# Kernel tuning notes

Measured on AMD Instinct MI355X. Metric: run time of the kernel, lower is better.

The kernel has to match this reference:

```python
import jax, jax.numpy as jnp
import numpy as np

DIM = 512
NUM_HEADS = 8
HEAD_DIM = DIM // NUM_HEADS
SCALE = HEAD_DIM ** -0.5


def setup_inputs() -> dict:
    key = jax.random.key(0)
    ks = jax.random.split(key, 10)
    B, Sq, Skv = 4, 2048, 2048
    std = DIM ** -0.5
    return {
        "x1": jax.random.normal(ks[0], (B, Sq, DIM), jnp.float32),
        "x2": jax.random.normal(ks[1], (B, Skv, DIM), jnp.float32),
        "Wq": jax.random.normal(ks[2], (DIM, DIM), jnp.float32) * std,
        "bq": jax.random.normal(ks[3], (DIM,), jnp.float32) * 0.02,
        "Wk": jax.random.normal(ks[4], (DIM, DIM), jnp.float32) * std,
        "bk": jax.random.normal(ks[5], (DIM,), jnp.float32) * 0.02,
        "Wv": jax.random.normal(ks[6], (DIM, DIM), jnp.float32) * std,
        "bv": jax.random.normal(ks[7], (DIM,), jnp.float32) * 0.02,
        "Wo": jax.random.normal(ks[8], (DIM, DIM), jnp.float32) * std,
        "bo": jax.random.normal(ks[9], (DIM,), jnp.float32) * 0.02,
    }


def reference(x1, x2, Wq, bq, Wk, bk, Wv, bv, Wo, bo):
    B, Sq, _ = x1.shape
    Skv = x2.shape[1]
    # Linear projections (torch nn.Linear: x @ W.T + b)
    Q = (x1 @ Wq.T + bq).reshape(B, Sq, NUM_HEADS, HEAD_DIM)
    K = (x2 @ Wk.T + bk).reshape(B, Skv, NUM_HEADS, HEAD_DIM)
    V = (x2 @ Wv.T + bv).reshape(B, Skv, NUM_HEADS, HEAD_DIM)
    # [B, H, Sq, Skv]
    attn = jnp.einsum("bqhd,bkhd->bhqk", Q, K) * SCALE
    attn = jax.nn.softmax(attn, axis=-1)  # dropout is identity in eval mode
    out = jnp.einsum("bhqk,bkhd->bqhd", attn, V).reshape(B, Sq, DIM)
    return out @ Wo.T + bo
```

## Files before the change

kernel.cpp:

```cpp
#include <hip/hip_runtime.h>
#include <math.h>

constexpr int kB = 4, kS = 2048, kDim = 512, kNH = 8, kHD = 64;
constexpr float kQScale = 0.18033688011112042f;

using bf16x8 = __attribute__((ext_vector_type(8))) short;
using f32x4  = __attribute__((ext_vector_type(4))) float;
using f32x16 = __attribute__((ext_vector_type(16))) float;

__device__ __forceinline__ unsigned pack_rn(float f0, float f1) {
  unsigned a = __builtin_bit_cast(unsigned, f0) + 0x8000u;
  unsigned b = __builtin_bit_cast(unsigned, f1) + 0x8000u;
  return __builtin_amdgcn_perm(b, a, 0x07060302u);
}
__device__ __forceinline__ unsigned short f2bf_rn(float f) {
  return (unsigned short)((__builtin_bit_cast(unsigned, f) + 0x8000u) >> 16);
}

#define GLDS(gp, lp) __builtin_amdgcn_global_load_lds(                         \
    (const __attribute__((address_space(1))) void*)(gp),                       \
    (__attribute__((address_space(3))) void*)(lp), 16, 0, 0)

__global__ __launch_bounds__(256) void cvt_bf16(
    const float* __restrict__ x1, const float* __restrict__ x2,
    const float* __restrict__ Wq, const float* __restrict__ Wk,
    const float* __restrict__ Wv, const float* __restrict__ Wo,
    unsigned short* __restrict__ x1b, unsigned short* __restrict__ x2b,
    unsigned short* __restrict__ wb) {
  const size_t i = (size_t)blockIdx.x * 256 + threadIdx.x;
  const float* src;
  unsigned short* dst;
  size_t off;
  if (i < 1048576) { src = x1; dst = x1b; off = i; }
  else if (i < 2097152) { src = x2; dst = x2b; off = i - 1048576; }
  else {
    const size_t j = i - 2097152;
    const int seg = (int)(j >> 16);
    src = seg == 0 ? Wq : seg == 1 ? Wk : seg == 2 ? Wv : Wo;
    dst = wb + (size_t)seg * 262144;
    off = j & 65535;
  }
  const float4 v = *(const float4*)(src + off * 4);
  uint2 o;
  o.x = pack_rn(v.x, v.y);
  o.y = pack_rn(v.z, v.w);
  *(uint2*)(dst + off * 4) = o;
}

__global__ __launch_bounds__(256) void qkv_gemm(
    const unsigned short* __restrict__ x1b, const unsigned short* __restrict__ x2b,
    const unsigned short* __restrict__ wb,
    const float* __restrict__ bq, const float* __restrict__ bk,
    const float* __restrict__ bv,
    unsigned short* __restrict__ Qg, unsigned short* __restrict__ Kg,
    unsigned short* __restrict__ Vg) {
  __shared__ __align__(16) short As[128 * 32];
  __shared__ __align__(16) short Bs[128 * 32];
  const int z = blockIdx.z;
  const unsigned short* X = z ? x2b : x1b;
  const unsigned short* W = wb + (size_t)z * (kDim * kDim);
  const float* bias = (z == 0) ? bq : (z == 1) ? bk : bv;

  const int t = threadIdx.x, lane = t & 63, w = t >> 6;
  const int g = lane >> 4, c = lane & 15;
  const int bm = blockIdx.y * 128, bn = blockIdx.x * 128;
  const int wm = (w >> 1) * 64, wn = (w & 1) * 64;
  const int lr = lane >> 2, lc = (lane & 3) * 8;

  f32x4 acc[4][4] = {};
  for (int k0 = 0; k0 < kDim; k0 += 32) {
    __syncthreads();
#pragma unroll
    for (int i = 0; i < 2; ++i) {
      const int ch = w * 2 + i;
      GLDS(X + (size_t)(bm + ch * 16 + lr) * kDim + k0 + lc, As + ch * 512);
      GLDS(W + (size_t)(bn + ch * 16 + lr) * kDim + k0 + lc, Bs + ch * 512);
    }
    __syncthreads();
    bf16x8 af[4], bfr[4];
#pragma unroll
    for (int tm = 0; tm < 4; ++tm) af[tm] = *(const bf16x8*)&As[(wm + tm * 16 + c) * 32 + g * 8];
#pragma unroll
    for (int tn = 0; tn < 4; ++tn) bfr[tn] = *(const bf16x8*)&Bs[(wn + tn * 16 + c) * 32 + g * 8];
#pragma unroll
    for (int tm = 0; tm < 4; ++tm)
#pragma unroll
      for (int tn = 0; tn < 4; ++tn)
        acc[tm][tn] = __builtin_amdgcn_mfma_f32_16x16x32_bf16(af[tm], bfr[tn], acc[tm][tn], 0, 0, 0);
  }

#pragma unroll
  for (int tm = 0; tm < 4; ++tm) {
#pragma unroll
    for (int tn = 0; tn < 4; ++tn) {
      const int n = bn + wn + tn * 16 + c;
      const float bb = bias[n];
      const int m0 = bm + wm + tm * 16 + g * 4;
      const float v0 = acc[tm][tn][0] + bb, v1 = acc[tm][tn][1] + bb;
      const float v2 = acc[tm][tn][2] + bb, v3 = acc[tm][tn][3] + bb;
      const int b_ = m0 >> 11, s0 = m0 & 2047;
      const int h_ = n >> 6, d_ = n & 63;
      const int bh = b_ * kNH + h_;
      if (z == 2) {
        uint2 pv;
        pv.x = pack_rn(v0, v1);
        pv.y = pack_rn(v2, v3);
        *(uint2*)(Vg + (((size_t)(bh * kHD + d_)) << 11) + s0) = pv;
      } else {
        const float sc = (z == 0) ? kQScale : 1.0f;
        unsigned short* dst = (z == 0 ? Qg : Kg) + (((size_t)(bh * kS + s0)) << 6) + d_;
        dst[0]   = f2bf_rn(v0 * sc);
        dst[64]  = f2bf_rn(v1 * sc);
        dst[128] = f2bf_rn(v2 * sc);
        dst[192] = f2bf_rn(v3 * sc);
      }
    }
  }
}

__global__ __launch_bounds__(256) void out_gemm(const unsigned short* __restrict__ A,
                                                const unsigned short* __restrict__ Wob,
                                                const float* __restrict__ bias,
                                                float* __restrict__ Y) {
  __shared__ __align__(16) short As[128 * 32];
  __shared__ __align__(16) short Bs[64 * 32];
  const int t = threadIdx.x, lane = t & 63, w = t >> 6;
  const int g = lane >> 4, c = lane & 15;
  const int bm = blockIdx.y * 128, bn = blockIdx.x * 64;
  const int lr = lane >> 2, lc = (lane & 3) * 8;

  f32x4 acc[2][4] = {};
  for (int k0 = 0; k0 < kDim; k0 += 32) {
    __syncthreads();
#pragma unroll
    for (int i = 0; i < 2; ++i) {
      const int ch = w * 2 + i;
      GLDS(A + (size_t)(bm + ch * 16 + lr) * kDim + k0 + lc, As + ch * 512);
    }
    GLDS(Wob + (size_t)(bn + w * 16 + lr) * kDim + k0 + lc, Bs + w * 512);
    __syncthreads();
    bf16x8 af[2], bfr[4];
#pragma unroll
    for (int tm = 0; tm < 2; ++tm) af[tm] = *(const bf16x8*)&As[(w * 32 + tm * 16 + c) * 32 + g * 8];
#pragma unroll
    for (int tn = 0; tn < 4; ++tn) bfr[tn] = *(const bf16x8*)&Bs[(tn * 16 + c) * 32 + g * 8];
#pragma unroll
    for (int tm = 0; tm < 2; ++tm)
#pragma unroll
      for (int tn = 0; tn < 4; ++tn)
        acc[tm][tn] = __builtin_amdgcn_mfma_f32_16x16x32_bf16(af[tm], bfr[tn], acc[tm][tn], 0, 0, 0);
  }
#pragma unroll
  for (int tm = 0; tm < 2; ++tm)
#pragma unroll
    for (int tn = 0; tn < 4; ++tn) {
      const int n = bn + tn * 16 + c;
      const float bb = bias[n];
      const int m0 = bm + w * 32 + tm * 16 + g * 4;
#pragma unroll
      for (int r = 0; r < 4; ++r)
        Y[(size_t)(m0 + r) * kDim + n] = acc[tm][tn][r] + bb;
    }
}

__global__ __launch_bounds__(256) void flash_mfma(const unsigned short* __restrict__ Qg,
                                                  const unsigned short* __restrict__ Kg,
                                                  const unsigned short* __restrict__ Vg,
                                                  unsigned short* __restrict__ attn) {
  __shared__ __align__(16) short Ks[64 * 76];
  __shared__ __align__(16) short Vs[64 * 76];
  const int t = threadIdx.x, lane = t & 63, w = t >> 6;
  const int c32 = lane & 31, g2 = lane >> 5;
  const int q0 = blockIdx.x * 128, bh = blockIdx.y, b_ = bh >> 3, h_ = bh & 7;

  const unsigned short* Qp = Qg + ((size_t)bh * kS + q0) * kHD;
  const unsigned short* Kp = Kg + (size_t)bh * kS * kHD;
  const unsigned short* Vp = Vg + (size_t)bh * kHD * kS;

  bf16x8 bq[4];
  {
    const unsigned short* qrow = Qp + (size_t)(w * 32 + c32) * kHD + g2 * 8;
#pragma unroll
    for (int ks = 0; ks < 4; ++ks) bq[ks] = *(const bf16x8*)(qrow + ks * 16);
  }

  const int r0 = t >> 3, cc0 = (t & 7) * 8;
  const unsigned short* kpt = Kp + (size_t)r0 * kHD + cc0;
  const unsigned short* vpt = Vp + (size_t)r0 * kS + cc0;
  uint4 pk0 = *(const uint4*)kpt;
  uint4 pk1 = *(const uint4*)(kpt + 32 * kHD);
  uint4 pv0 = *(const uint4*)vpt;
  uint4 pv1 = *(const uint4*)(vpt + 32 * kS);
  kpt += 64 * kHD;
  vpt += 64;

  float l = 0.f;
  f32x16 o0 = {}, o1 = {};

  for (int kv0 = 0; kv0 < kS; kv0 += 64) {
    __syncthreads();
    *(uint4*)&Ks[r0 * 76 + cc0] = pk0;
    *(uint4*)&Ks[(r0 + 32) * 76 + cc0] = pk1;
    *(uint4*)&Vs[r0 * 76 + cc0] = pv0;
    *(uint4*)&Vs[(r0 + 32) * 76 + cc0] = pv1;
    if (kv0 + 64 < kS) {
      pk0 = *(const uint4*)kpt;
      pk1 = *(const uint4*)(kpt + 32 * kHD);
      pv0 = *(const uint4*)vpt;
      pv1 = *(const uint4*)(vpt + 32 * kS);
      kpt += 64 * kHD;
      vpt += 64;
    }
    __syncthreads();

    f32x16 sa0 = {}, sa1 = {};
#pragma unroll
    for (int ks = 0; ks < 4; ++ks) {
      const bf16x8 a0 = *(const bf16x8*)&Ks[c32 * 76 + ks * 16 + g2 * 8];
      const bf16x8 a1 = *(const bf16x8*)&Ks[(32 + c32) * 76 + ks * 16 + g2 * 8];
      sa0 = __builtin_amdgcn_mfma_f32_32x32x16_bf16(a0, bq[ks], sa0, 0, 0, 0);
      sa1 = __builtin_amdgcn_mfma_f32_32x32x16_bf16(a1, bq[ks], sa1, 0, 0, 0);
    }

    uint2 pk8[8];
#pragma unroll
    for (int kt = 0; kt < 2; ++kt) {
      const f32x16 sv = kt ? sa1 : sa0;
#pragma unroll
      for (int rg = 0; rg < 4; ++rg) {
        const float p0 = exp2f(sv[rg * 4 + 0]);
        const float p1 = exp2f(sv[rg * 4 + 1]);
        const float p2 = exp2f(sv[rg * 4 + 2]);
        const float p3 = exp2f(sv[rg * 4 + 3]);
        l += (p0 + p1) + (p2 + p3);
        pk8[kt * 4 + rg].x = pack_rn(p0, p1);
        pk8[kt * 4 + rg].y = pack_rn(p2, p3);
      }
    }

#pragma unroll
    for (int kvs = 0; kvs < 4; ++kvs) {
      const int base = (kvs >> 1) * 4 + (kvs & 1) * 2;
      const uint2 own = g2 ? pk8[base + 1] : pk8[base];
      const uint2 snd = g2 ? pk8[base] : pk8[base + 1];
      uint2 rcv;
      rcv.x = (unsigned)__shfl_xor((int)snd.x, 32, 64);
      rcv.y = (unsigned)__shfl_xor((int)snd.y, 32, 64);
      uint4 bfr;
      bfr.x = g2 ? rcv.x : own.x;
      bfr.y = g2 ? rcv.y : own.y;
      bfr.z = g2 ? own.x : rcv.x;
      bfr.w = g2 ? own.y : rcv.y;
      const bf16x8 bp = __builtin_bit_cast(bf16x8, bfr);
      const bf16x8 v0 = *(const bf16x8*)&Vs[c32 * 76 + kvs * 16 + g2 * 8];
      const bf16x8 v1 = *(const bf16x8*)&Vs[(32 + c32) * 76 + kvs * 16 + g2 * 8];
      o0 = __builtin_amdgcn_mfma_f32_32x32x16_bf16(v0, bp, o0, 0, 0, 0);
      o1 = __builtin_amdgcn_mfma_f32_32x32x16_bf16(v1, bp, o1, 0, 0, 0);
    }
  }

  l += __shfl_xor(l, 32, 64);
  const float inv = 1.0f / l;
  unsigned short* orow = attn + ((size_t)b_ * kS + q0 + w * 32 + c32) * kDim + h_ * kHD;
#pragma unroll
  for (int dt = 0; dt < 2; ++dt) {
    const f32x16 oo = dt ? o1 : o0;
#pragma unroll
    for (int rg = 0; rg < 4; ++rg) {
      uint2 st;
      st.x = pack_rn(oo[rg * 4 + 0] * inv, oo[rg * 4 + 1] * inv);
      st.y = pack_rn(oo[rg * 4 + 2] * inv, oo[rg * 4 + 3] * inv);
      *(uint2*)(orow + dt * 32 + 8 * rg + 4 * g2) = st;
    }
  }
}

extern "C" void kernel_launch(void* const* d_in, const int* in_sizes, int n_in,
                              void* d_out, int out_size, void* d_ws, size_t ws_size,
                              hipStream_t stream) {
  const float* x1 = (const float*)d_in[0];
  const float* x2 = (const float*)d_in[1];
  const float* Wq = (const float*)d_in[2];
  const float* bq = (const float*)d_in[3];
  const float* Wk = (const float*)d_in[4];
  const float* bk = (const float*)d_in[5];
  const float* Wv = (const float*)d_in[6];
  const float* bv = (const float*)d_in[7];
  const float* Wo = (const float*)d_in[8];
  const float* bo = (const float*)d_in[9];
  float* out = (float*)d_out;

  constexpr size_t kTok = (size_t)kB * kS * kDim;
  unsigned short* x1b = (unsigned short*)d_ws;
  unsigned short* x2b = x1b + kTok;
  unsigned short* wb  = x2b + kTok;
  unsigned short* Qg  = wb + 4 * (size_t)(kDim * kDim);
  unsigned short* Kg  = Qg + kTok;
  unsigned short* Vg  = Kg + kTok;
  unsigned short* atb = Vg + kTok;

  const dim3 blk(256);
  cvt_bf16<<<dim3(9216), blk, 0, stream>>>(x1, x2, Wq, Wk, Wv, Wo, x1b, x2b, wb);
  qkv_gemm<<<dim3(4, 64, 3), blk, 0, stream>>>(x1b, x2b, wb, bq, bk, bv, Qg, Kg, Vg);
  flash_mfma<<<dim3(16, 32), blk, 0, stream>>>(Qg, Kg, Vg, atb);
  out_gemm<<<dim3(8, 64), blk, 0, stream>>>(atb, wb + 3 * (size_t)(kDim * kDim), bo, out);
}
```

Before: 200.1 us.

## Widen GEMM K-step, permute K rows to drop P shuffles, reorder flash grid

```diff
diff --git a/kernel.cpp b/kernel.cpp
--- a/kernel.cpp
+++ b/kernel.cpp
@@ -54,8 +54,8 @@
     const float* __restrict__ bv,
     unsigned short* __restrict__ Qg, unsigned short* __restrict__ Kg,
     unsigned short* __restrict__ Vg) {
-  __shared__ __align__(16) short As[128 * 32];
-  __shared__ __align__(16) short Bs[128 * 32];
+  __shared__ __align__(16) short As0[128 * 32], As1[128 * 32];
+  __shared__ __align__(16) short Bs0[128 * 32], Bs1[128 * 32];
   const int z = blockIdx.z;
   const unsigned short* X = z ? x2b : x1b;
   const unsigned short* W = wb + (size_t)z * (kDim * kDim);
@@ -68,25 +68,34 @@
   const int lr = lane >> 2, lc = (lane & 3) * 8;
 
   f32x4 acc[4][4] = {};
-  for (int k0 = 0; k0 < kDim; k0 += 32) {
+  for (int k0 = 0; k0 < kDim; k0 += 64) {
     __syncthreads();
 #pragma unroll
     for (int i = 0; i < 2; ++i) {
-      const int ch = w * 2 + i;
-      GLDS(X + (size_t)(bm + ch * 16 + lr) * kDim + k0 + lc, As + ch * 512);
-      GLDS(W + (size_t)(bn + ch * 16 + lr) * kDim + k0 + lc, Bs + ch * 512);
-    }
-    __syncthreads();
-    bf16x8 af[4], bfr[4];
-#pragma unroll
-    for (int tm = 0; tm < 4; ++tm) af[tm] = *(const bf16x8*)&As[(wm + tm * 16 + c) * 32 + g * 8];
-#pragma unroll
-    for (int tn = 0; tn < 4; ++tn) bfr[tn] = *(const bf16x8*)&Bs[(wn + tn * 16 + c) * 32 + g * 8];
-#pragma unroll
-    for (int tm = 0; tm < 4; ++tm)
-#pragma unroll
-      for (int tn = 0; tn < 4; ++tn)
-        acc[tm][tn] = __builtin_amdgcn_mfma_f32_16x16x32_bf16(af[tm], bfr[tn], acc[tm][tn], 0, 0, 0);
+      const int row = i * 64 + w * 16;
+      const size_t ga = (size_t)(bm + row + lr) * kDim + k0 + lc;
+      const size_t gb = (size_t)(bn + row + lr) * kDim + k0 + lc;
+      GLDS(X + ga, As0 + row * 32);
+      GLDS(X + ga + 32, As1 + row * 32);
+      GLDS(W + gb, Bs0 + row * 32);
+      GLDS(W + gb + 32, Bs1 + row * 32);
+    }
+    __syncthreads();
+#pragma unroll
+    for (int kk = 0; kk < 2; ++kk) {
+      const short* Ap = kk ? As1 : As0;
+      const short* Bp = kk ? Bs1 : Bs0;
+      bf16x8 af[4], bfr[4];
+#pragma unroll
+      for (int tm = 0; tm < 4; ++tm) af[tm] = *(const bf16x8*)&Ap[(wm + tm * 16 + c) * 32 + g * 8];
+#pragma unroll
+      for (int tn = 0; tn < 4; ++tn) bfr[tn] = *(const bf16x8*)&Bp[(wn + tn * 16 + c) * 32 + g * 8];
+#pragma unroll
+      for (int tm = 0; tm < 4; ++tm)
+#pragma unroll
+        for (int tn = 0; tn < 4; ++tn)
+          acc[tm][tn] = __builtin_amdgcn_mfma_f32_16x16x32_bf16(af[tm], bfr[tn], acc[tm][tn], 0, 0, 0);
+    }
   }
 
 #pragma unroll
@@ -122,33 +131,45 @@
                                                 const unsigned short* __restrict__ Wob,
                                                 const float* __restrict__ bias,
                                                 float* __restrict__ Y) {
-  __shared__ __align__(16) short As[128 * 32];
-  __shared__ __align__(16) short Bs[64 * 32];
+  __shared__ __align__(16) short As0[128 * 32], As1[128 * 32];
+  __shared__ __align__(16) short Bs0[64 * 32], Bs1[64 * 32];
   const int t = threadIdx.x, lane = t & 63, w = t >> 6;
   const int g = lane >> 4, c = lane & 15;
   const int bm = blockIdx.y * 128, bn = blockIdx.x * 64;
   const int lr = lane >> 2, lc = (lane & 3) * 8;
 
   f32x4 acc[2][4] = {};
-  for (int k0 = 0; k0 < kDim; k0 += 32) {
+  for (int k0 = 0; k0 < kDim; k0 += 64) {
     __syncthreads();
 #pragma unroll
     for (int i = 0; i < 2; ++i) {
-      const int ch = w * 2 + i;
-      GLDS(A + (size_t)(bm + ch * 16 + lr) * kDim + k0 + lc, As + ch * 512);
-    }
-    GLDS(Wob + (size_t)(bn + w * 16 + lr) * kDim + k0 + lc, Bs + w * 512);
-    __syncthreads();
-    bf16x8 af[2], bfr[4];
-#pragma unroll
-    for (int tm = 0; tm < 2; ++tm) af[tm] = *(const bf16x8*)&As[(w * 32 + tm * 16 + c) * 32 + g * 8];
-#pragma unroll
-    for (int tn = 0; tn < 4; ++tn) bfr[tn] = *(const bf16x8*)&Bs[(tn * 16 + c) * 32 + g * 8];
-#pragma unroll
-    for (int tm = 0; tm < 2; ++tm)
-#pragma unroll
-      for (int tn = 0; tn < 4; ++tn)
-        acc[tm][tn] = __builtin_amdgcn_mfma_f32_16x16x32_bf16(af[tm], bfr[tn], acc[tm][tn], 0, 0, 0);
+      const int row = i * 64 + w * 16;
+      const size_t ga = (size_t)(bm + row + lr) * kDim + k0 + lc;
+      GLDS(A + ga, As0 + row * 32);
+      GLDS(A + ga + 32, As1 + row * 32);
+    }
+    {
+      const int row = w * 16;
+      const size_t gb = (size_t)(bn + row + lr) * kDim + k0 + lc;
+      GLDS(Wob + gb, Bs0 + row * 32);
+      GLDS(Wob + gb + 32, Bs1 + row * 32);
+    }
+    __syncthreads();
+#pragma unroll
+    for (int kk = 0; kk < 2; ++kk) {
+      const short* Ap = kk ? As1 : As0;
+      const short* Bp = kk ? Bs1 : Bs0;
+      bf16x8 af[2], bfr[4];
+#pragma unroll
+      for (int tm = 0; tm < 2; ++tm) af[tm] = *(const bf16x8*)&Ap[(w * 32 + tm * 16 + c) * 32 + g * 8];
+#pragma unroll
+      for (int tn = 0; tn < 4; ++tn) bfr[tn] = *(const bf16x8*)&Bp[(tn * 16 + c) * 32 + g * 8];
+#pragma unroll
+      for (int tm = 0; tm < 2; ++tm)
+#pragma unroll
+        for (int tn = 0; tn < 4; ++tn)
+          acc[tm][tn] = __builtin_amdgcn_mfma_f32_16x16x32_bf16(af[tm], bfr[tn], acc[tm][tn], 0, 0, 0);
+    }
   }
 #pragma unroll
   for (int tm = 0; tm < 2; ++tm)
@@ -171,7 +192,7 @@
   __shared__ __align__(16) short Vs[64 * 76];
   const int t = threadIdx.x, lane = t & 63, w = t >> 6;
   const int c32 = lane & 31, g2 = lane >> 5;
-  const int q0 = blockIdx.x * 128, bh = blockIdx.y, b_ = bh >> 3, h_ = bh & 7;
+  const int bh = blockIdx.x, q0 = blockIdx.y * 128, b_ = bh >> 3, h_ = bh & 7;
 
   const unsigned short* Qp = Qg + ((size_t)bh * kS + q0) * kHD;
   const unsigned short* Kp = Kg + (size_t)bh * kS * kHD;
@@ -185,6 +206,7 @@
   }
 
   const int r0 = t >> 3, cc0 = (t & 7) * 8;
+  const int pr = r0 ^ ((((r0 >> 2) ^ (r0 >> 3)) & 1) * 12);
   const unsigned short* kpt = Kp + (size_t)r0 * kHD + cc0;
   const unsigned short* vpt = Vp + (size_t)r0 * kS + cc0;
   uint4 pk0 = *(const uint4*)kpt;
@@ -199,8 +221,8 @@
 
   for (int kv0 = 0; kv0 < kS; kv0 += 64) {
     __syncthreads();
-    *(uint4*)&Ks[r0 * 76 + cc0] = pk0;
-    *(uint4*)&Ks[(r0 + 32) * 76 + cc0] = pk1;
+    *(uint4*)&Ks[pr * 76 + cc0] = pk0;
+    *(uint4*)&Ks[(pr + 32) * 76 + cc0] = pk1;
     *(uint4*)&Vs[r0 * 76 + cc0] = pv0;
     *(uint4*)&Vs[(r0 + 32) * 76 + cc0] = pv1;
     if (kv0 + 64 < kS) {
@@ -222,40 +244,32 @@
       sa1 = __builtin_amdgcn_mfma_f32_32x32x16_bf16(a1, bq[ks], sa1, 0, 0, 0);
     }
 
-    uint2 pk8[8];
+    uint4 bp[4];
 #pragma unroll
     for (int kt = 0; kt < 2; ++kt) {
       const f32x16 sv = kt ? sa1 : sa0;
 #pragma unroll
-      for (int rg = 0; rg < 4; ++rg) {
-        const float p0 = exp2f(sv[rg * 4 + 0]);
-        const float p1 = exp2f(sv[rg * 4 + 1]);
-        const float p2 = exp2f(sv[rg * 4 + 2]);
-        const float p3 = exp2f(sv[rg * 4 + 3]);
-        l += (p0 + p1) + (p2 + p3);
-        pk8[kt * 4 + rg].x = pack_rn(p0, p1);
-        pk8[kt * 4 + rg].y = pack_rn(p2, p3);
+      for (int h = 0; h < 2; ++h) {
+        float p[8];
+#pragma unroll
+        for (int j = 0; j < 8; ++j) p[j] = exp2f(sv[h * 8 + j]);
+        l += ((p[0] + p[1]) + (p[2] + p[3])) + ((p[4] + p[5]) + (p[6] + p[7]));
+        uint4 pk;
+        pk.x = pack_rn(p[0], p[1]);
+        pk.y = pack_rn(p[2], p[3]);
+        pk.z = pack_rn(p[4], p[5]);
+        pk.w = pack_rn(p[6], p[7]);
+        bp[kt * 2 + h] = pk;
       }
     }
 
 #pragma unroll
     for (int kvs = 0; kvs < 4; ++kvs) {
-      const int base = (kvs >> 1) * 4 + (kvs & 1) * 2;
-      const uint2 own = g2 ? pk8[base + 1] : pk8[base];
-      const uint2 snd = g2 ? pk8[base] : pk8[base + 1];
-      uint2 rcv;
-      rcv.x = (unsigned)__shfl_xor((int)snd.x, 32, 64);
-      rcv.y = (unsigned)__shfl_xor((int)snd.y, 32, 64);
-      uint4 bfr;
-      bfr.x = g2 ? rcv.x : own.x;
-      bfr.y = g2 ? rcv.y : own.y;
-      bfr.z = g2 ? own.x : rcv.x;
-      bfr.w = g2 ? own.y : rcv.y;
-      const bf16x8 bp = __builtin_bit_cast(bf16x8, bfr);
+      const bf16x8 bpf = __builtin_bit_cast(bf16x8, bp[kvs]);
       const bf16x8 v0 = *(const bf16x8*)&Vs[c32 * 76 + kvs * 16 + g2 * 8];
       const bf16x8 v1 = *(const bf16x8*)&Vs[(32 + c32) * 76 + kvs * 16 + g2 * 8];
-      o0 = __builtin_amdgcn_mfma_f32_32x32x16_bf16(v0, bp, o0, 0, 0, 0);
-      o1 = __builtin_amdgcn_mfma_f32_32x32x16_bf16(v1, bp, o1, 0, 0, 0);
+      o0 = __builtin_amdgcn_mfma_f32_32x32x16_bf16(v0, bpf, o0, 0, 0, 0);
+      o1 = __builtin_amdgcn_mfma_f32_32x32x16_bf16(v1, bpf, o1, 0, 0, 0);
     }
   }
 
@@ -302,6 +316,6 @@
   const dim3 blk(256);
   cvt_bf16<<<dim3(9216), blk, 0, stream>>>(x1, x2, Wq, Wk, Wv, Wo, x1b, x2b, wb);
   qkv_gemm<<<dim3(4, 64, 3), blk, 0, stream>>>(x1b, x2b, wb, bq, bk, bv, Qg, Kg, Vg);
-  flash_mfma<<<dim3(16, 32), blk, 0, stream>>>(Qg, Kg, Vg, atb);
+  flash_mfma<<<dim3(32, 16), blk, 0, stream>>>(Qg, Kg, Vg, atb);
   out_gemm<<<dim3(8, 64), blk, 0, stream>>>(atb, wb + 3 * (size_t)(kDim * kDim), bo, out);
 }
```

Measured after the change: 196.1 us. 1.02x faster.
